# Kernel optimization log

Hardware: AMD Instinct MI355X
Metric: run time of the kernel (lower is better)

Reference implementation:

```python
import jax, jax.numpy as jnp
import numpy as np

EMBED_DIM = 200
INPUT_DIM = 512


def setup_inputs() -> dict:
    key = jax.random.key(0)
    k1, k2, k3, k4 = jax.random.split(key, 4)
    B, L, T = 64, 256, 64
    x = jax.random.normal(k1, (B, L, INPUT_DIM), dtype=jnp.float32)
    y = jax.random.normal(k2, (B, T, INPUT_DIM), dtype=jnp.float32)
    # fc = nn.Linear(input_dim, embedding_dim)
    W = jax.random.normal(k3, (EMBED_DIM, INPUT_DIM), dtype=jnp.float32) * (1.0 / np.sqrt(INPUT_DIM))
    b = jax.random.normal(k4, (EMBED_DIM,), dtype=jnp.float32) * 0.01
    return {"x": x, "y": y, "W": W, "b": b}


def reference(x, y, W, b):
    # Project both modalities (last dim != embedding_dim in original triggers fc)
    xp = jnp.einsum('bld,ed->ble', x, W) + b   # B x L x E
    yp = jnp.einsum('btd,ed->bte', y, W) + b   # B x T x E
    # Pairwise matchmap: for pair (i, j), matchmap = xp[i] @ yp[j].T -> L x T
    mm = jnp.einsum('ile,jte->ijlt', xp, yp)   # B x B x L x T
    # MISA: max over L (rows of matchmap, dim 0), then mean over T
    S = jnp.max(mm, axis=2).mean(axis=2)       # B x B
    return S
```

## Files before the change

kernel.cpp:

```cpp
#include <hip/hip_runtime.h>
#include <hip/hip_bf16.h>
#include <stdint.h>

#define BB 64
#define LL 256
#define TT 64
#define DD 512
#define EE 200
#define EP 208
#define NKK 13
#define NROWS_X 16384
#define BSTRIDE 264

typedef __attribute__((ext_vector_type(8))) short short8;
typedef __attribute__((ext_vector_type(4))) float floatx4;
typedef __attribute__((ext_vector_type(16))) float floatx16;

__device__ __forceinline__ short f2bf(float f) {
  uint32_t u = __builtin_bit_cast(uint32_t, f);
  u = (u + 0x7fffu + ((u >> 16) & 1u)) >> 16;
  return (short)u;
}

__device__ __forceinline__ uint32_t pack2(float lo, float hi) {
  return __builtin_amdgcn_perm(__builtin_bit_cast(uint32_t, hi),
                               __builtin_bit_cast(uint32_t, lo), 0x07060302u);
}

typedef const __attribute__((address_space(1))) uint32_t gu32_t;
typedef __attribute__((address_space(3))) uint32_t lu32_t;
__device__ __forceinline__ void glds16(const void* g, void* l) {
  __builtin_amdgcn_global_load_lds((gu32_t*)g, (lu32_t*)l, 16, 0, 0);
}

__global__ void wcvt_kernel(const float* __restrict__ W, short* __restrict__ Wb) {
  const int t = blockIdx.x * 256 + threadIdx.x;
  const int base = t * 8;
  const int e = base >> 9;
  short8 o;
  if (e < EE) {
    const floatx4 f0 = *(const floatx4*)(W + base);
    const floatx4 f1 = *(const floatx4*)(W + base + 4);
    o[0] = f2bf(f0.x); o[1] = f2bf(f0.y); o[2] = f2bf(f0.z); o[3] = f2bf(f0.w);
    o[4] = f2bf(f1.x); o[5] = f2bf(f1.y); o[6] = f2bf(f1.z); o[7] = f2bf(f1.w);
  } else {
    o = (short8)0;
  }
  *(short8*)(Wb + base) = o;
}

__global__ __launch_bounds__(256, 3) void proj_kernel(const float* __restrict__ x,
                                                      const float* __restrict__ y,
                                                      const short* __restrict__ Wb,
                                                      const float* __restrict__ bias,
                                                      short* __restrict__ pT) {
  __shared__ __align__(16) char smem[43008];
  float* ldsA = (float*)smem;
  short* ldsB = (short*)(smem + 16384);
  short* bounce = (short*)smem;

  const int tid  = threadIdx.x;
  const int lane = tid & 63;
  const int wid  = tid >> 6;
  const int r16   = lane & 15;
  const int khalf = lane >> 4;

  const int row0 = blockIdx.x * 64;
  const float* srcbase = (row0 < NROWS_X) ? (x + (size_t)row0 * DD)
                                          : (y + (size_t)(row0 - NROWS_X) * DD);

  floatx4 acc[NKK];
#pragma unroll
  for (int n = 0; n < NKK; n++) acc[n] = (floatx4){0.f, 0.f, 0.f, 0.f};

  auto stage = [&](int buf, int ks) {
#pragma unroll
    for (int it = 0; it < 2; it++) {
      const int p = it * 256 + tid;
      const int r = p >> 3, c = p & 7;
      glds16(srcbase + (size_t)r * DD + ks * 32 + ((c ^ (r & 7)) << 2),
             &ldsA[buf * 2048 + p * 4]);
    }
#pragma unroll
    for (int it = 0; it < 4; it++) {
      const int p = it * 256 + tid;
      if (p < 832) {
        const int r = p >> 2, c = p & 3;
        glds16(Wb + (size_t)r * DD + ks * 32 + ((c ^ (r & 3)) << 3),
               &ldsB[buf * 6656 + p * 8]);
      }
    }
  };

  stage(0, 0);

  for (int s = 0; s < 16; s++) {
    __syncthreads();
    if (s + 1 < 16) stage((s + 1) & 1, s + 1);

    const int buf = s & 1;
    const int r = wid * 16 + r16;
    const int c0 = (2 * khalf) ^ (r & 7);
    const int c1 = (2 * khalf + 1) ^ (r & 7);
    const floatx4 f0 = *(const floatx4*)&ldsA[buf * 2048 + r * 32 + c0 * 4];
    const floatx4 f1 = *(const floatx4*)&ldsA[buf * 2048 + r * 32 + c1 * 4];
    union { short8 s8; uint32_t u[4]; } af;
    af.u[0] = pack2(f0.x, f0.y);
    af.u[1] = pack2(f0.z, f0.w);
    af.u[2] = pack2(f1.x, f1.y);
    af.u[3] = pack2(f1.z, f1.w);
#pragma unroll
    for (int n = 0; n < NKK; n++) {
      const int erow = n * 16 + r16;
      const short8 bfrag = *(const short8*)&ldsB[buf * 6656 + erow * 32 + ((khalf ^ (erow & 3)) << 3)];
      acc[n] = __builtin_amdgcn_mfma_f32_16x16x32_bf16(af.s8, bfrag, acc[n], 0, 0, 0);
    }
  }

  __syncthreads();

#pragma unroll
  for (int n = 0; n < NKK; n++) {
    const int e = n * 16 + r16;
    const float bv = (e < EE) ? bias[e] : 0.0f;
#pragma unroll
    for (int rr = 0; rr < 4; rr++) {
      const int lr = wid * 16 + khalf * 4 + rr;
      bounce[lr * BSTRIDE + e] = f2bf(acc[n][rr] + bv);
    }
  }
  __syncthreads();

  const int rowblk0 = row0 >> 5;
  for (int c = tid; c < 1664; c += 256) {
    const int q  = c >> 6;
    const int mt = (q >= 13) ? 1 : 0;
    const int n  = q - mt * 13;
    const int l  = c & 63;
    const int lr = mt * 32 + (l & 31);
    const short8 piece = *(const short8*)&bounce[lr * BSTRIDE + n * 16 + (l >> 5) * 8];
    *(short8*)&pT[((size_t)((rowblk0 + mt) * 13 + n)) * 512 + l * 8] = piece;
  }
}

__global__ __launch_bounds__(512, 2) void pair_kernel(const short* __restrict__ xpT,
                                                      const short* __restrict__ ypT,
                                                      float* __restrict__ S) {
  __shared__ __align__(16) char lds[2 * 53248 + 16384];
  float* red = (float*)(lds + 2 * 53248);

  const int tid  = threadIdx.x;
  const int lane = tid & 63;
  const int wid  = tid >> 6;
  const int jj2  = wid >> 2;
  const int wj   = wid & 3;
  const int bid  = blockIdx.x;
  const int i    = bid & 63;
  const int jq   = bid >> 6;
  const int jbase = jq * 16;

  short8 a0[NKK], a1[NKK];
  {
    const short* ab0 = xpT + ((size_t)((i * 8 + wj * 2 + 0) * NKK)) * 512 + lane * 8;
    const short* ab1 = xpT + ((size_t)((i * 8 + wj * 2 + 1) * NKK)) * 512 + lane * 8;
#pragma unroll
    for (int kk = 0; kk < NKK; kk++) {
      a0[kk] = *(const short8*)(ab0 + kk * 512);
      a1[kk] = *(const short8*)(ab1 + kk * 512);
    }
  }

  auto stageB = [&](int g) {
    const short* src = ypT + (size_t)(jbase + g * 2) * 26 * 512;
    char* dst = lds + (g & 1) * 53248;
    for (int c = tid; c < 3328; c += 512)
      glds16(src + (size_t)c * 8, dst + c * 16);
  };

  stageB(0);
  __syncthreads();

  for (int g = 0; g < 8; g++) {
    if (g + 1 < 8) stageB(g + 1);

    const int j = g * 2 + jj2;
    const short* bbase = (const short*)(lds + (g & 1) * 53248) +
                         (size_t)(jj2 * 26 * 512) + lane * 8;

    floatx16 accA0n0, accA0n1, accA1n0, accA1n1;
#pragma unroll
    for (int r = 0; r < 16; r++) {
      accA0n0[r] = 0.f; accA0n1[r] = 0.f; accA1n0[r] = 0.f; accA1n1[r] = 0.f;
    }

#pragma unroll
    for (int kk = 0; kk < NKK; kk++) {
      const short8 b0 = *(const short8*)(bbase + (0 * NKK + kk) * 512);
      const short8 b1 = *(const short8*)(bbase + (1 * NKK + kk) * 512);
      accA0n0 = __builtin_amdgcn_mfma_f32_32x32x16_bf16(a0[kk], b0, accA0n0, 0, 0, 0);
      accA1n0 = __builtin_amdgcn_mfma_f32_32x32x16_bf16(a1[kk], b0, accA1n0, 0, 0, 0);
      accA0n1 = __builtin_amdgcn_mfma_f32_32x32x16_bf16(a0[kk], b1, accA0n1, 0, 0, 0);
      accA1n1 = __builtin_amdgcn_mfma_f32_32x32x16_bf16(a1[kk], b1, accA1n1, 0, 0, 0);
    }

    float v0 = accA0n0[0], v1 = accA0n1[0];
#pragma unroll
    for (int r = 0; r < 16; r++) {
      v0 = fmaxf(v0, accA0n0[r]); v0 = fmaxf(v0, accA1n0[r]);
      v1 = fmaxf(v1, accA0n1[r]); v1 = fmaxf(v1, accA1n1[r]);
    }
    v0 = fmaxf(v0, __shfl_xor(v0, 32, 64));
    v1 = fmaxf(v1, __shfl_xor(v1, 32, 64));
    if (lane < 32) {
      red[(j * 4 + wj) * 64 + 0 * 32 + lane] = v0;
      red[(j * 4 + wj) * 64 + 1 * 32 + lane] = v1;
    }

    __syncthreads();
  }

#pragma unroll
  for (int rep = 0; rep < 2; rep++) {
    const int j = wid * 2 + rep;
    const int t = lane;
    float v = red[(j * 4 + 0) * 64 + t];
    v = fmaxf(v, red[(j * 4 + 1) * 64 + t]);
    v = fmaxf(v, red[(j * 4 + 2) * 64 + t]);
    v = fmaxf(v, red[(j * 4 + 3) * 64 + t]);
    v += __shfl_xor(v, 1, 64);
    v += __shfl_xor(v, 2, 64);
    v += __shfl_xor(v, 4, 64);
    v += __shfl_xor(v, 8, 64);
    v += __shfl_xor(v, 16, 64);
    v += __shfl_xor(v, 32, 64);
    if (t == 0) S[i * BB + jbase + j] = v * (1.0f / 64.0f);
  }
}

extern "C" void kernel_launch(void* const* d_in, const int* in_sizes, int n_in,
                              void* d_out, int out_size, void* d_ws, size_t ws_size,
                              hipStream_t stream) {
  const float* x = (const float*)d_in[0];
  const float* y = (const float*)d_in[1];
  const float* W = (const float*)d_in[2];
  const float* b = (const float*)d_in[3];
  float* S = (float*)d_out;

  char* ws = (char*)d_ws;
  short* Wb = (short*)ws;
  short* pT = (short*)(ws + 262144);
  short* ypT = pT + (size_t)6656 * 512;

  wcvt_kernel<<<52, 256, 0, stream>>>(W, Wb);
  proj_kernel<<<320, 256, 0, stream>>>(x, y, Wb, b, pT);
  pair_kernel<<<256, 512, 0, stream>>>(pT, ypT, S);
}
```

Before: 47.92 us.

## Halve proj_kernel row tile and split embedding columns across waves

The projection kernel now handles 32 rows per block instead of 64 and launches 640 blocks. The four waves are arranged as 2 row-groups by 2 embedding halves (7 and 6 MFMA tiles each). The goal is more blocks to fill the CUs and higher occupancy, helped by smaller LDS and fewer accumulators (launch bounds raised to 4). The cost is that each W tile in LDS is reused across half as many rows, so more W traffic per output row, and the B-fragment swizzle was changed to match.

```diff
diff --git a/kernel.cpp b/kernel.cpp
--- a/kernel.cpp
+++ b/kernel.cpp
@@ -49,14 +49,14 @@
   *(short8*)(Wb + base) = o;
 }
 
-__global__ __launch_bounds__(256, 3) void proj_kernel(const float* __restrict__ x,
+__global__ __launch_bounds__(256, 4) void proj_kernel(const float* __restrict__ x,
                                                       const float* __restrict__ y,
                                                       const short* __restrict__ Wb,
                                                       const float* __restrict__ bias,
                                                       short* __restrict__ pT) {
-  __shared__ __align__(16) char smem[43008];
+  __shared__ __align__(16) char smem[34816];
   float* ldsA = (float*)smem;
-  short* ldsB = (short*)(smem + 16384);
+  short* ldsB = (short*)(smem + 8192);
   short* bounce = (short*)smem;
 
   const int tid  = threadIdx.x;
@@ -64,29 +64,30 @@
   const int wid  = tid >> 6;
   const int r16   = lane & 15;
   const int khalf = lane >> 4;
-
-  const int row0 = blockIdx.x * 64;
+  const int mw = wid >> 1;
+  const int eh = wid & 1;
+
+  const int row0 = blockIdx.x * 32;
   const float* srcbase = (row0 < NROWS_X) ? (x + (size_t)row0 * DD)
                                           : (y + (size_t)(row0 - NROWS_X) * DD);
 
-  floatx4 acc[NKK];
-#pragma unroll
-  for (int n = 0; n < NKK; n++) acc[n] = (floatx4){0.f, 0.f, 0.f, 0.f};
+  floatx4 acc[7];
+#pragma unroll
+  for (int n = 0; n < 7; n++) acc[n] = (floatx4){0.f, 0.f, 0.f, 0.f};
 
   auto stage = [&](int buf, int ks) {
-#pragma unroll
-    for (int it = 0; it < 2; it++) {
-      const int p = it * 256 + tid;
+    {
+      const int p = tid;
       const int r = p >> 3, c = p & 7;
       glds16(srcbase + (size_t)r * DD + ks * 32 + ((c ^ (r & 7)) << 2),
-             &ldsA[buf * 2048 + p * 4]);
+             &ldsA[buf * 1024 + p * 4]);
     }
 #pragma unroll
     for (int it = 0; it < 4; it++) {
       const int p = it * 256 + tid;
       if (p < 832) {
         const int r = p >> 2, c = p & 3;
-        glds16(Wb + (size_t)r * DD + ks * 32 + ((c ^ (r & 3)) << 3),
+        glds16(Wb + (size_t)r * DD + ks * 32 + ((c ^ ((r >> 1) & 3)) << 3),
                &ldsB[buf * 6656 + p * 8]);
       }
     }
@@ -99,47 +100,57 @@
     if (s + 1 < 16) stage((s + 1) & 1, s + 1);
 
     const int buf = s & 1;
-    const int r = wid * 16 + r16;
-    const int c0 = (2 * khalf) ^ (r & 7);
-    const int c1 = (2 * khalf + 1) ^ (r & 7);
-    const floatx4 f0 = *(const floatx4*)&ldsA[buf * 2048 + r * 32 + c0 * 4];
-    const floatx4 f1 = *(const floatx4*)&ldsA[buf * 2048 + r * 32 + c1 * 4];
+    const int r = mw * 16 + r16;
+    const int c0 = (2 * khalf) ^ (r16 & 7);
+    const int c1 = (2 * khalf + 1) ^ (r16 & 7);
+    const floatx4 f0 = *(const floatx4*)&ldsA[buf * 1024 + r * 32 + c0 * 4];
+    const floatx4 f1 = *(const floatx4*)&ldsA[buf * 1024 + r * 32 + c1 * 4];
     union { short8 s8; uint32_t u[4]; } af;
     af.u[0] = pack2(f0.x, f0.y);
     af.u[1] = pack2(f0.z, f0.w);
     af.u[2] = pack2(f1.x, f1.y);
     af.u[3] = pack2(f1.z, f1.w);
-#pragma unroll
-    for (int n = 0; n < NKK; n++) {
-      const int erow = n * 16 + r16;
-      const short8 bfrag = *(const short8*)&ldsB[buf * 6656 + erow * 32 + ((khalf ^ (erow & 3)) << 3)];
-      acc[n] = __builtin_amdgcn_mfma_f32_16x16x32_bf16(af.s8, bfrag, acc[n], 0, 0, 0);
+    const int bcol = (khalf ^ ((r16 >> 1) & 3)) << 3;
+    if (eh == 0) {
+#pragma unroll
+      for (int nn = 0; nn < 7; nn++) {
+        const int erow = nn * 16 + r16;
+        const short8 bfrag = *(const short8*)&ldsB[buf * 6656 + erow * 32 + bcol];
+        acc[nn] = __builtin_amdgcn_mfma_f32_16x16x32_bf16(af.s8, bfrag, acc[nn], 0, 0, 0);
+      }
+    } else {
+#pragma unroll
+      for (int nn = 0; nn < 6; nn++) {
+        const int erow = (7 + nn) * 16 + r16;
+        const short8 bfrag = *(const short8*)&ldsB[buf * 6656 + erow * 32 + bcol];
+        acc[nn] = __builtin_amdgcn_mfma_f32_16x16x32_bf16(af.s8, bfrag, acc[nn], 0, 0, 0);
+      }
     }
   }
 
   __syncthreads();
 
-#pragma unroll
-  for (int n = 0; n < NKK; n++) {
-    const int e = n * 16 + r16;
-    const float bv = (e < EE) ? bias[e] : 0.0f;
-#pragma unroll
-    for (int rr = 0; rr < 4; rr++) {
-      const int lr = wid * 16 + khalf * 4 + rr;
-      bounce[lr * BSTRIDE + e] = f2bf(acc[n][rr] + bv);
+  {
+    const int ncnt = 7 - eh;
+    const int nbase = eh * 7;
+    for (int nn = 0; nn < ncnt; nn++) {
+      const int e = (nbase + nn) * 16 + r16;
+      const float bv = (e < EE) ? bias[e] : 0.0f;
+#pragma unroll
+      for (int rr = 0; rr < 4; rr++) {
+        const int lr = mw * 16 + khalf * 4 + rr;
+        bounce[lr * BSTRIDE + e] = f2bf(acc[nn][rr] + bv);
+      }
     }
   }
   __syncthreads();
 
-  const int rowblk0 = row0 >> 5;
-  for (int c = tid; c < 1664; c += 256) {
-    const int q  = c >> 6;
-    const int mt = (q >= 13) ? 1 : 0;
-    const int n  = q - mt * 13;
-    const int l  = c & 63;
-    const int lr = mt * 32 + (l & 31);
-    const short8 piece = *(const short8*)&bounce[lr * BSTRIDE + n * 16 + (l >> 5) * 8];
-    *(short8*)&pT[((size_t)((rowblk0 + mt) * 13 + n)) * 512 + l * 8] = piece;
+  const int rowblk0 = blockIdx.x;
+  for (int c = tid; c < 832; c += 256) {
+    const int n = c >> 6;
+    const int l = c & 63;
+    const short8 piece = *(const short8*)&bounce[(l & 31) * BSTRIDE + n * 16 + (l >> 5) * 8];
+    *(short8*)&pT[((size_t)(rowblk0 * 13 + n)) * 512 + l * 8] = piece;
   }
 }
 
@@ -252,6 +263,6 @@
   short* ypT = pT + (size_t)6656 * 512;
 
   wcvt_kernel<<<52, 256, 0, stream>>>(W, Wb);
-  proj_kernel<<<320, 256, 0, stream>>>(x, y, Wb, b, pT);
+  proj_kernel<<<640, 256, 0, stream>>>(x, y, Wb, b, pT);
   pair_kernel<<<256, 512, 0, stream>>>(pT, ypT, S);
 }
```

After: 48.53 us. About the same (+1.3%).
